# Kernel optimization log

Hardware: AMD Instinct MI355X
Metric: run time of the kernel (lower is better)

Reference implementation:

```python
import jax, jax.numpy as jnp
import numpy as np

B = 16384          # batch
F = 64             # number of feature columns (tables)
L = 10             # pooled lookups per feature (bag size)
E = 16             # embedding dim
V = 1_000_000      # hashed vocab size (shared table)
D = F * E          # concat width = 1024
EPS = 1e-5


def setup_inputs() -> dict:
    key = jax.random.key(0)
    ks = jax.random.split(key, 9)
    idx = jax.random.randint(ks[0], (B, F, L), 0, V, dtype=jnp.int64)
    # NormalTensorInitializer(var=0.01) -> std 0.1
    emb = jax.random.normal(ks[1], (V, E), dtype=jnp.float32) * 0.1
    W1 = jax.random.normal(ks[2], (D, 1024), dtype=jnp.float32) / np.sqrt(D).astype(np.float32)
    b1 = jnp.zeros((1024,), jnp.float32)
    W2 = jax.random.normal(ks[3], (1024, 512), dtype=jnp.float32) / np.sqrt(1024).astype(np.float32)
    b2 = jnp.zeros((512,), jnp.float32)
    W3 = jax.random.normal(ks[4], (512, 1), dtype=jnp.float32) / np.sqrt(512).astype(np.float32)
    b3 = jnp.zeros((1,), jnp.float32)
    return {"idx": idx, "emb": emb, "W1": W1, "b1": b1,
            "W2": W2, "b2": b2, "W3": W3, "b3": b3}


def reference(idx, emb, W1, b1, W2, b2, W3, b3):
    # EmbeddingSumConcat: gather [B,F,L,E], sum-pool over bag dim, concat features
    pooled = jnp.take(emb, idx, axis=0).sum(axis=2)          # [B, F, E]
    x = pooled.reshape(B, D)                                  # [B, F*E]
    # ms.nn.Normalization: per-feature batch standardization
    mu = x.mean(axis=0, keepdims=True)
    var = x.var(axis=0, keepdims=True)
    x = (x - mu) * jax.lax.rsqrt(var + EPS)
    # Dense tower 1024 -> 1024 -> 512 -> 1, sigmoid
    h = jax.nn.relu(x @ W1 + b1)
    h = jax.nn.relu(h @ W2 + b2)
    out = jax.nn.sigmoid(h @ W3 + b3)                         # [B, 1]
    return out
```

## Files before the change

kernel.cpp:

```cpp
#include <hip/hip_runtime.h>
#include <hip/hip_bf16.h>
#include <math.h>

typedef __attribute__((ext_vector_type(8))) short  short8;
typedef __attribute__((ext_vector_type(4))) float  f32x4;
typedef __attribute__((ext_vector_type(4))) unsigned short u16x4;
typedef __attribute__((ext_vector_type(8))) unsigned short u16x8;

#define BATCH 16384
#define NF    64
#define BAGL  10
#define ED    16
#define DW    1024
#define VOCAB 1000000

static __device__ __forceinline__ unsigned short f2bf(float f) {
    unsigned int u = __builtin_bit_cast(unsigned int, f);
    unsigned int r = (u + 0x7fffu + ((u >> 16) & 1u)) >> 16;
    return (unsigned short)r;
}
static __device__ __forceinline__ float bf2f(unsigned short h) {
    unsigned int u = ((unsigned int)h) << 16;
    return __builtin_bit_cast(float, u);
}

__global__ __launch_bounds__(256) void emb_to_bf16(const float* __restrict__ e,
                                                   unsigned short* __restrict__ o) {
    const long long i = ((long long)blockIdx.x * 256 + threadIdx.x) * 8;
    if (i >= (long long)VOCAB * ED) return;
    const f32x4 a = *(const f32x4*)(e + i);
    const f32x4 b = *(const f32x4*)(e + i + 4);
    u16x8 r;
#pragma unroll
    for (int j = 0; j < 4; ++j) { r[j] = f2bf(a[j]); r[4 + j] = f2bf(b[j]); }
    *(u16x8*)(o + i) = r;
}

__global__ __launch_bounds__(256) void pool_bf16(const int* __restrict__ idx,
                                                 const unsigned short* __restrict__ embb,
                                                 unsigned short* __restrict__ xb) {
    const int gid = blockIdx.x * 256 + threadIdx.x;
    const int bag = gid >> 1;
    const int h   = gid & 1;
    const int* ip = idx + (long long)bag * BAGL;

    int v[BAGL];
#pragma unroll
    for (int l = 0; l < BAGL; ++l) v[l] = ip[l];
    u16x8 e[BAGL];
#pragma unroll
    for (int l = 0; l < BAGL; ++l)
        e[l] = *(const u16x8*)(embb + (((long long)v[l]) << 4) + h * 8);

    float s[8] = {0, 0, 0, 0, 0, 0, 0, 0};
#pragma unroll
    for (int l = 0; l < BAGL; ++l)
#pragma unroll
        for (int j = 0; j < 8; ++j) s[j] += bf2f(e[l][j]);

    u16x8 o;
#pragma unroll
    for (int j = 0; j < 8; ++j) o[j] = f2bf(s[j]);
    *(u16x8*)(xb + (((long long)bag) << 4) + h * 8) = o;
}

__global__ __launch_bounds__(256) void stats_kernel(const unsigned short* __restrict__ xb,
                                                    float* __restrict__ ssum,
                                                    float* __restrict__ ssq) {
    const int t = threadIdx.x;
    const long long r0 = (long long)blockIdx.x * 128;
    float s[4] = {0, 0, 0, 0}, q[4] = {0, 0, 0, 0};
    for (int r = 0; r < 128; ++r) {
        const u16x4 v = *(const u16x4*)(xb + (r0 + r) * DW + t * 4);
#pragma unroll
        for (int j = 0; j < 4; ++j) { float f = bf2f(v[j]); s[j] += f; q[j] += f * f; }
    }
#pragma unroll
    for (int j = 0; j < 4; ++j) {
        atomicAdd(&ssum[t * 4 + j], s[j]);
        atomicAdd(&ssq [t * 4 + j], q[j]);
    }
}

__global__ void finalize_stats(const float* __restrict__ ssum, const float* __restrict__ ssq,
                               float* __restrict__ mean, float* __restrict__ rsig,
                               float* __restrict__ murs) {
    const int c = blockIdx.x * 256 + threadIdx.x;
    const float m = ssum[c] * (1.0f / (float)BATCH);
    const float v = ssq[c] * (1.0f / (float)BATCH) - m * m;
    const float r = rsqrtf(v + 1e-5f);
    mean[c] = m; rsig[c] = r; murs[c] = m * r;
}

template <int SCALE>
__global__ __launch_bounds__(256) void transpose_f32_bf16(const float* __restrict__ src,
                                                          unsigned short* __restrict__ dst,
                                                          int R, int C,
                                                          const float* __restrict__ rs) {
    __shared__ float tile[32][33];
    const int tx = threadIdx.x & 31, ty = threadIdx.x >> 5;
    const int bx = blockIdx.x, by = blockIdx.y;
#pragma unroll
    for (int i = 0; i < 4; ++i) {
        const int r = by * 32 + ty + i * 8, c = bx * 32 + tx;
        float v = src[(long long)r * C + c];
        if (SCALE) v *= rs[r];
        tile[ty + i * 8][tx] = v;
    }
    __syncthreads();
#pragma unroll
    for (int i = 0; i < 4; ++i) {
        const int oc = bx * 32 + ty + i * 8;
        dst[(long long)oc * R + by * 32 + tx] = f2bf(tile[tx][ty + i * 8]);
    }
}

__global__ __launch_bounds__(256) void b1fold_kernel(const float* __restrict__ W1,
                                                     const float* __restrict__ murs,
                                                     float* __restrict__ b1n) {
    const int n = blockIdx.x * 256 + threadIdx.x;
    const int k0 = blockIdx.y * 128;
    float acc = 0.f;
#pragma unroll 4
    for (int k = 0; k < 128; ++k)
        acc += murs[k0 + k] * W1[(long long)(k0 + k) * 1024 + n];
    atomicAdd(&b1n[n], -acc);
}

__global__ __launch_bounds__(256) void gemm_relu(const unsigned short* __restrict__ A,
                                                 const unsigned short* __restrict__ Bt,
                                                 const float* __restrict__ bias,
                                                 const float* __restrict__ bias2,
                                                 unsigned short* __restrict__ C,
                                                 int M, int N, int K, int NBN) {
    __shared__ __align__(16) unsigned short As[128 * 64];
    __shared__ __align__(16) unsigned short Bs[128 * 64];
    const int tid = threadIdx.x;
    const int w = tid >> 6, l = tid & 63;
    const int wr = w >> 1, wc = w & 1;
    const int blk = blockIdx.x, xcd = blk & 7, j = blk >> 3;
    const int bm = xcd * 16 + j / NBN, bn = j % NBN;
    const int l15 = l & 15, l4 = l >> 4;

    f32x4 acc[4][4] = {};
    const long long a_base = (long long)bm * 128 * K;
    const long long b_base = (long long)bn * 128 * K;

    for (int k0 = 0; k0 < K; k0 += 64) {
#pragma unroll
        for (int i = 0; i < 4; ++i) {
            const int cid = i * 256 + tid;
            const int row = cid >> 3, kq = (cid & 7) << 3;
            __builtin_amdgcn_global_load_lds(
                (const __attribute__((address_space(1))) void*)(A + a_base + (long long)row * K + k0 + kq),
                (__attribute__((address_space(3))) void*)(&As[cid * 8]), 16, 0, 0);
            __builtin_amdgcn_global_load_lds(
                (const __attribute__((address_space(1))) void*)(Bt + b_base + (long long)row * K + k0 + kq),
                (__attribute__((address_space(3))) void*)(&Bs[cid * 8]), 16, 0, 0);
        }
        __syncthreads();

        short8 a[2][4], b[2][4];
#pragma unroll
        for (int kk = 0; kk < 2; ++kk) {
#pragma unroll
            for (int m = 0; m < 4; ++m)
                a[kk][m] = *(const short8*)(As + (wr * 64 + m * 16 + l15) * 64 + kk * 32 + l4 * 8);
#pragma unroll
            for (int n = 0; n < 4; ++n)
                b[kk][n] = *(const short8*)(Bs + (wc * 64 + n * 16 + l15) * 64 + kk * 32 + l4 * 8);
        }
#pragma unroll
        for (int kk = 0; kk < 2; ++kk)
#pragma unroll
            for (int m = 0; m < 4; ++m)
#pragma unroll
                for (int n = 0; n < 4; ++n)
                    acc[m][n] = __builtin_amdgcn_mfma_f32_16x16x32_bf16(a[kk][m], b[kk][n], acc[m][n], 0, 0, 0);
        __syncthreads();
    }

#pragma unroll
    for (int m = 0; m < 4; ++m) {
        const int grow_base = bm * 128 + wr * 64 + m * 16 + l4 * 4;
#pragma unroll
        for (int n = 0; n < 4; ++n) {
            const int gcol = bn * 128 + wc * 64 + n * 16 + l15;
            const float bv = bias[gcol] + (bias2 ? bias2[gcol] : 0.f);
#pragma unroll
            for (int j2 = 0; j2 < 4; ++j2) {
                float v = fmaxf(acc[m][n][j2] + bv, 0.f);
                C[(long long)(grow_base + j2) * N + gcol] = f2bf(v);
            }
        }
    }
}

__global__ __launch_bounds__(256) void gemm2_fused(const unsigned short* __restrict__ A,
                                                   const unsigned short* __restrict__ Bt,
                                                   const float* __restrict__ bias,
                                                   const float* __restrict__ W3,
                                                   float* __restrict__ logits,
                                                   int M, int N, int K, int NBN) {
    __shared__ __align__(16) unsigned short As[128 * 64];
    __shared__ __align__(16) unsigned short Bs[128 * 64];
    const int tid = threadIdx.x;
    const int w = tid >> 6, l = tid & 63;
    const int wr = w >> 1, wc = w & 1;
    const int blk = blockIdx.x, xcd = blk & 7, j = blk >> 3;
    const int bm = xcd * 16 + j / NBN, bn = j % NBN;
    const int l15 = l & 15, l4 = l >> 4;

    f32x4 acc[4][4] = {};
    const long long a_base = (long long)bm * 128 * K;
    const long long b_base = (long long)bn * 128 * K;

    for (int k0 = 0; k0 < K; k0 += 64) {
#pragma unroll
        for (int i = 0; i < 4; ++i) {
            const int cid = i * 256 + tid;
            const int row = cid >> 3, kq = (cid & 7) << 3;
            __builtin_amdgcn_global_load_lds(
                (const __attribute__((address_space(1))) void*)(A + a_base + (long long)row * K + k0 + kq),
                (__attribute__((address_space(3))) void*)(&As[cid * 8]), 16, 0, 0);
            __builtin_amdgcn_global_load_lds(
                (const __attribute__((address_space(1))) void*)(Bt + b_base + (long long)row * K + k0 + kq),
                (__attribute__((address_space(3))) void*)(&Bs[cid * 8]), 16, 0, 0);
        }
        __syncthreads();

        short8 a[2][4], b[2][4];
#pragma unroll
        for (int kk = 0; kk < 2; ++kk) {
#pragma unroll
            for (int m = 0; m < 4; ++m)
                a[kk][m] = *(const short8*)(As + (wr * 64 + m * 16 + l15) * 64 + kk * 32 + l4 * 8);
#pragma unroll
            for (int n = 0; n < 4; ++n)
                b[kk][n] = *(const short8*)(Bs + (wc * 64 + n * 16 + l15) * 64 + kk * 32 + l4 * 8);
        }
#pragma unroll
        for (int kk = 0; kk < 2; ++kk)
#pragma unroll
            for (int m = 0; m < 4; ++m)
#pragma unroll
                for (int n = 0; n < 4; ++n)
                    acc[m][n] = __builtin_amdgcn_mfma_f32_16x16x32_bf16(a[kk][m], b[kk][n], acc[m][n], 0, 0, 0);
        __syncthreads();
    }

#pragma unroll
    for (int m = 0; m < 4; ++m) {
        float part[4] = {0.f, 0.f, 0.f, 0.f};
#pragma unroll
        for (int n = 0; n < 4; ++n) {
            const int gcol = bn * 128 + wc * 64 + n * 16 + l15;
            const float bv = bias[gcol];
            const float w3 = W3[gcol];
#pragma unroll
            for (int j2 = 0; j2 < 4; ++j2) {
                float v = fmaxf(acc[m][n][j2] + bv, 0.f);
                part[j2] += v * w3;
            }
        }
#pragma unroll
        for (int off = 1; off < 16; off <<= 1)
#pragma unroll
            for (int j2 = 0; j2 < 4; ++j2) part[j2] += __shfl_xor(part[j2], off, 64);
        if (l15 == 0) {
            const int grow = bm * 128 + wr * 64 + m * 16 + l4 * 4;
#pragma unroll
            for (int j2 = 0; j2 < 4; ++j2) atomicAdd(&logits[grow + j2], part[j2]);
        }
    }
}

__global__ __launch_bounds__(256) void sigmoid_kernel(const float* __restrict__ logits,
                                                      const float* __restrict__ b3,
                                                      float* __restrict__ out) {
    const int i = blockIdx.x * 256 + threadIdx.x;
    out[i] = 1.0f / (1.0f + expf(-(logits[i] + b3[0])));
}

extern "C" void kernel_launch(void* const* d_in, const int* in_sizes, int n_in,
                              void* d_out, int out_size, void* d_ws, size_t ws_size,
                              hipStream_t stream) {
    const int*   idx = (const int*)d_in[0];
    const float* emb = (const float*)d_in[1];
    const float* W1  = (const float*)d_in[2];
    const float* b1  = (const float*)d_in[3];
    const float* W2  = (const float*)d_in[4];
    const float* b2  = (const float*)d_in[5];
    const float* W3  = (const float*)d_in[6];
    const float* b3  = (const float*)d_in[7];
    float* out = (float*)d_out;

    const size_t EMBB_H1_BYTES = (size_t)BATCH * DW * 2;

    char* ws = (char*)d_ws;
    unsigned short* xb   = (unsigned short*)ws; ws += (size_t)BATCH * DW * 2;
    unsigned short* embb = (unsigned short*)ws; ws += EMBB_H1_BYTES;
    unsigned short* h1   = embb;
    unsigned short* w1t  = (unsigned short*)ws; ws += (size_t)1024 * 1024 * 2;
    unsigned short* w2t  = (unsigned short*)ws; ws += (size_t)512 * 1024 * 2;
    float* ssum   = (float*)ws; ws += 4096;
    float* ssq    = (float*)ws; ws += 4096;
    float* b1n    = (float*)ws; ws += 4096;
    float* logits = (float*)ws; ws += (size_t)BATCH * 4;
    float* mean   = (float*)ws; ws += 4096;
    float* rsig   = (float*)ws; ws += 4096;
    float* murs   = (float*)ws; ws += 4096;

    hipMemsetAsync(ssum, 0, 4096 * 3 + (size_t)BATCH * 4, stream);

    const long long embElems = (long long)VOCAB * ED;
    const int embBlocks = (int)((embElems / 8 + 255) / 256);
    emb_to_bf16<<<embBlocks, 256, 0, stream>>>(emb, embb);
    pool_bf16<<<(BATCH * NF * 2) / 256, 256, 0, stream>>>(idx, embb, xb);
    stats_kernel<<<BATCH / 128, 256, 0, stream>>>(xb, ssum, ssq);
    finalize_stats<<<4, 256, 0, stream>>>(ssum, ssq, mean, rsig, murs);

    transpose_f32_bf16<1><<<dim3(32, 32), 256, 0, stream>>>(W1, w1t, 1024, 1024, rsig);
    b1fold_kernel<<<dim3(4, 8), 256, 0, stream>>>(W1, murs, b1n);
    transpose_f32_bf16<0><<<dim3(16, 32), 256, 0, stream>>>(W2, w2t, 1024, 512, nullptr);

    gemm_relu<<<(BATCH / 128) * (1024 / 128), 256, 0, stream>>>(
        xb, w1t, b1, b1n, h1, BATCH, 1024, 1024, 1024 / 128);
    gemm2_fused<<<(BATCH / 128) * (512 / 128), 256, 0, stream>>>(
        h1, w2t, b2, W3, logits, BATCH, 512, 1024, 512 / 128);

    sigmoid_kernel<<<BATCH / 256, 256, 0, stream>>>(logits, b3, out);
}
```

Before: 325.8 us.

## Double-buffer GEMM LDS tiles with async prefetch and XOR swizzle

Rewrites the shared GEMM main loop for both dense layers to double-buffer the A/B tiles in LDS. The tile two steps ahead is issued with global_load_lds while MFMAs run on the current tile, synchronised by explicit vmcnt waits and barriers. It also adds an XOR swizzle on the LDS column chunks to reduce bank conflicts, raises MFMA wave priority, and requests two blocks per CU. The risks are doubled LDS use (64KB per block) limiting occupancy, and the hand-placed waitcnt logic being fragile. bias2 is now read unconditionally, so it must never be null.

```diff
diff --git a/kernel.cpp b/kernel.cpp
--- a/kernel.cpp
+++ b/kernel.cpp
@@ -127,58 +127,85 @@
     atomicAdd(&b1n[n], -acc);
 }
 
-__global__ __launch_bounds__(256) void gemm_relu(const unsigned short* __restrict__ A,
-                                                 const unsigned short* __restrict__ Bt,
-                                                 const float* __restrict__ bias,
-                                                 const float* __restrict__ bias2,
-                                                 unsigned short* __restrict__ C,
-                                                 int M, int N, int K, int NBN) {
-    __shared__ __align__(16) unsigned short As[128 * 64];
-    __shared__ __align__(16) unsigned short Bs[128 * 64];
-    const int tid = threadIdx.x;
-    const int w = tid >> 6, l = tid & 63;
-    const int wr = w >> 1, wc = w & 1;
+#define GEMM_STAGE(dstA, dstB, kt)                                              \
+  {                                                                             \
+    const int k0s = (kt) * 64;                                                  \
+    _Pragma("unroll")                                                           \
+    for (int g = 0; g < 4; ++g) {                                               \
+      const int cid = g * 256 + tid;                                            \
+      const int rr = cid >> 3, pos = cid & 7;                                   \
+      const int csrc = (pos ^ (rr & 7)) << 3;                                   \
+      __builtin_amdgcn_global_load_lds(                                         \
+        (const __attribute__((address_space(1))) void*)(A + a_base + (long long)rr * K + k0s + csrc), \
+        (__attribute__((address_space(3))) void*)(&(dstA)[cid * 8]), 16, 0, 0); \
+      __builtin_amdgcn_global_load_lds(                                         \
+        (const __attribute__((address_space(1))) void*)(Bt + b_base + (long long)rr * K + k0s + csrc), \
+        (__attribute__((address_space(3))) void*)(&(dstB)[cid * 8]), 16, 0, 0); \
+    }                                                                           \
+  }
+
+#define GEMM_CORE_LOOP                                                          \
+    const int tid = threadIdx.x;                                                \
+    const int w = tid >> 6, l = tid & 63;                                       \
+    const int wr = w >> 1, wc = w & 1;                                          \
+    const int l15 = l & 15, l4 = l >> 4;                                        \
+    f32x4 acc[4][4] = {};                                                       \
+    const long long a_base = (long long)bm * 128 * K;                           \
+    const long long b_base = (long long)bn * 128 * K;                           \
+    const int NT = K >> 6;                                                      \
+    GEMM_STAGE(As[0], Bs[0], 0)                                                 \
+    GEMM_STAGE(As[1], Bs[1], 1)                                                 \
+    asm volatile("s_waitcnt vmcnt(8)" ::: "memory");                            \
+    __builtin_amdgcn_sched_barrier(0);                                          \
+    __builtin_amdgcn_s_barrier();                                               \
+    for (int t = 0; t < NT; ++t) {                                              \
+        const unsigned short* Ap = As[t & 1];                                   \
+        const unsigned short* Bp = Bs[t & 1];                                   \
+        short8 a[2][4], b[2][4];                                                \
+        _Pragma("unroll")                                                       \
+        for (int kk = 0; kk < 2; ++kk) {                                        \
+            const int swz = ((kk * 4 + l4) ^ (l15 & 7)) << 3;                   \
+            _Pragma("unroll")                                                   \
+            for (int m = 0; m < 4; ++m)                                         \
+                a[kk][m] = *(const short8*)(Ap + (wr * 64 + m * 16 + l15) * 64 + swz); \
+            _Pragma("unroll")                                                   \
+            for (int n = 0; n < 4; ++n)                                         \
+                b[kk][n] = *(const short8*)(Bp + (wc * 64 + n * 16 + l15) * 64 + swz); \
+        }                                                                       \
+        asm volatile("s_waitcnt lgkmcnt(0)" ::: "memory");                      \
+        __builtin_amdgcn_sched_barrier(0);                                      \
+        __builtin_amdgcn_s_barrier();                                           \
+        if (t + 2 < NT) { GEMM_STAGE(As[t & 1], Bs[t & 1], t + 2) }             \
+        __builtin_amdgcn_s_setprio(1);                                          \
+        _Pragma("unroll")                                                       \
+        for (int kk = 0; kk < 2; ++kk)                                          \
+            _Pragma("unroll")                                                   \
+            for (int m = 0; m < 4; ++m)                                         \
+                _Pragma("unroll")                                               \
+                for (int n = 0; n < 4; ++n)                                     \
+                    acc[m][n] = __builtin_amdgcn_mfma_f32_16x16x32_bf16(        \
+                        a[kk][m], b[kk][n], acc[m][n], 0, 0, 0);                \
+        __builtin_amdgcn_s_setprio(0);                                          \
+        if (t + 1 < NT) {                                                       \
+            if (t + 2 < NT) { asm volatile("s_waitcnt vmcnt(8)" ::: "memory"); }\
+            else            { asm volatile("s_waitcnt vmcnt(0)" ::: "memory"); }\
+            __builtin_amdgcn_sched_barrier(0);                                  \
+            __builtin_amdgcn_s_barrier();                                       \
+        }                                                                       \
+    }
+
+__global__ __launch_bounds__(256, 2) void gemm_relu(const unsigned short* __restrict__ A,
+                                                    const unsigned short* __restrict__ Bt,
+                                                    const float* __restrict__ bias,
+                                                    const float* __restrict__ bias2,
+                                                    unsigned short* __restrict__ C,
+                                                    int M, int N, int K, int NBN) {
+    __shared__ __align__(16) unsigned short As[2][128 * 64];
+    __shared__ __align__(16) unsigned short Bs[2][128 * 64];
     const int blk = blockIdx.x, xcd = blk & 7, j = blk >> 3;
     const int bm = xcd * 16 + j / NBN, bn = j % NBN;
-    const int l15 = l & 15, l4 = l >> 4;
-
-    f32x4 acc[4][4] = {};
-    const long long a_base = (long long)bm * 128 * K;
-    const long long b_base = (long long)bn * 128 * K;
-
-    for (int k0 = 0; k0 < K; k0 += 64) {
-#pragma unroll
-        for (int i = 0; i < 4; ++i) {
-            const int cid = i * 256 + tid;
-            const int row = cid >> 3, kq = (cid & 7) << 3;
-            __builtin_amdgcn_global_load_lds(
-                (const __attribute__((address_space(1))) void*)(A + a_base + (long long)row * K + k0 + kq),
-                (__attribute__((address_space(3))) void*)(&As[cid * 8]), 16, 0, 0);
-            __builtin_amdgcn_global_load_lds(
-                (const __attribute__((address_space(1))) void*)(Bt + b_base + (long long)row * K + k0 + kq),
-                (__attribute__((address_space(3))) void*)(&Bs[cid * 8]), 16, 0, 0);
-        }
-        __syncthreads();
-
-        short8 a[2][4], b[2][4];
-#pragma unroll
-        for (int kk = 0; kk < 2; ++kk) {
-#pragma unroll
-            for (int m = 0; m < 4; ++m)
-                a[kk][m] = *(const short8*)(As + (wr * 64 + m * 16 + l15) * 64 + kk * 32 + l4 * 8);
-#pragma unroll
-            for (int n = 0; n < 4; ++n)
-                b[kk][n] = *(const short8*)(Bs + (wc * 64 + n * 16 + l15) * 64 + kk * 32 + l4 * 8);
-        }
-#pragma unroll
-        for (int kk = 0; kk < 2; ++kk)
-#pragma unroll
-            for (int m = 0; m < 4; ++m)
-#pragma unroll
-                for (int n = 0; n < 4; ++n)
-                    acc[m][n] = __builtin_amdgcn_mfma_f32_16x16x32_bf16(a[kk][m], b[kk][n], acc[m][n], 0, 0, 0);
-        __syncthreads();
-    }
+
+    GEMM_CORE_LOOP
 
 #pragma unroll
     for (int m = 0; m < 4; ++m) {
@@ -186,7 +213,7 @@
 #pragma unroll
         for (int n = 0; n < 4; ++n) {
             const int gcol = bn * 128 + wc * 64 + n * 16 + l15;
-            const float bv = bias[gcol] + (bias2 ? bias2[gcol] : 0.f);
+            const float bv = bias[gcol] + bias2[gcol];
 #pragma unroll
             for (int j2 = 0; j2 < 4; ++j2) {
                 float v = fmaxf(acc[m][n][j2] + bv, 0.f);
@@ -196,58 +223,18 @@
     }
 }
 
-__global__ __launch_bounds__(256) void gemm2_fused(const unsigned short* __restrict__ A,
-                                                   const unsigned short* __restrict__ Bt,
-                                                   const float* __restrict__ bias,
-                                                   const float* __restrict__ W3,
-                                                   float* __restrict__ logits,
-                                                   int M, int N, int K, int NBN) {
-    __shared__ __align__(16) unsigned short As[128 * 64];
-    __shared__ __align__(16) unsigned short Bs[128 * 64];
-    const int tid = threadIdx.x;
-    const int w = tid >> 6, l = tid & 63;
-    const int wr = w >> 1, wc = w & 1;
+__global__ __launch_bounds__(256, 2) void gemm2_fused(const unsigned short* __restrict__ A,
+                                                      const unsigned short* __restrict__ Bt,
+                                                      const float* __restrict__ bias,
+                                                      const float* __restrict__ W3,
+                                                      float* __restrict__ logits,
+                                                      int M, int N, int K, int NBN) {
+    __shared__ __align__(16) unsigned short As[2][128 * 64];
+    __shared__ __align__(16) unsigned short Bs[2][128 * 64];
     const int blk = blockIdx.x, xcd = blk & 7, j = blk >> 3;
     const int bm = xcd * 16 + j / NBN, bn = j % NBN;
-    const int l15 = l & 15, l4 = l >> 4;
-
-    f32x4 acc[4][4] = {};
-    const long long a_base = (long long)bm * 128 * K;
-    const long long b_base = (long long)bn * 128 * K;
-
-    for (int k0 = 0; k0 < K; k0 += 64) {
-#pragma unroll
-        for (int i = 0; i < 4; ++i) {
-            const int cid = i * 256 + tid;
-            const int row = cid >> 3, kq = (cid & 7) << 3;
-            __builtin_amdgcn_global_load_lds(
-                (const __attribute__((address_space(1))) void*)(A + a_base + (long long)row * K + k0 + kq),
-                (__attribute__((address_space(3))) void*)(&As[cid * 8]), 16, 0, 0);
-            __builtin_amdgcn_global_load_lds(
-                (const __attribute__((address_space(1))) void*)(Bt + b_base + (long long)row * K + k0 + kq),
-                (__attribute__((address_space(3))) void*)(&Bs[cid * 8]), 16, 0, 0);
-        }
-        __syncthreads();
-
-        short8 a[2][4], b[2][4];
-#pragma unroll
-        for (int kk = 0; kk < 2; ++kk) {
-#pragma unroll
-            for (int m = 0; m < 4; ++m)
-                a[kk][m] = *(const short8*)(As + (wr * 64 + m * 16 + l15) * 64 + kk * 32 + l4 * 8);
-#pragma unroll
-            for (int n = 0; n < 4; ++n)
-                b[kk][n] = *(const short8*)(Bs + (wc * 64 + n * 16 + l15) * 64 + kk * 32 + l4 * 8);
-        }
-#pragma unroll
-        for (int kk = 0; kk < 2; ++kk)
-#pragma unroll
-            for (int m = 0; m < 4; ++m)
-#pragma unroll
-                for (int n = 0; n < 4; ++n)
-                    acc[m][n] = __builtin_amdgcn_mfma_f32_16x16x32_bf16(a[kk][m], b[kk][n], acc[m][n], 0, 0, 0);
-        __syncthreads();
-    }
+
+    GEMM_CORE_LOOP
 
 #pragma unroll
     for (int m = 0; m < 4; ++m) {
```

After: 295.5 us. 1.1x faster.
